# Optimization experiments

Measured on AMD Instinct MI355X. Metric: run time of the kernel, lower is better.

Reference implementation:

```python
import jax, jax.numpy as jnp
import numpy as np

N_SAM, N_GEN, N_E = 10000, 20000, 1000000
D_SAM, D_GEN = 2000, 500
D0, H = 256, [256, 128, 64]
SLOPE = 0.25


def _glorot(key, shape):
    fan_in, fan_out = shape
    s = jnp.sqrt(2.0 / (fan_in + fan_out))
    return jax.random.normal(key, shape, dtype=jnp.float32) * s


def setup_inputs() -> dict:
    key = jax.random.key(0)
    ks = jax.random.split(key, 24)
    inp = {
        "sam_feat": jax.random.normal(ks[0], (N_SAM, D_SAM), dtype=jnp.float32),
        "gen_feat": jax.random.normal(ks[1], (N_GEN, D_GEN), dtype=jnp.float32),
        "src_sg": jax.random.randint(ks[2], (N_E,), 0, N_SAM, dtype=jnp.int32),
        "dst_sg": jax.random.randint(ks[3], (N_E,), 0, N_GEN, dtype=jnp.int32),
        "src_gs": jax.random.randint(ks[4], (N_E,), 0, N_GEN, dtype=jnp.int32),
        "dst_gs": jax.random.randint(ks[5], (N_E,), 0, N_SAM, dtype=jnp.int32),
        # input projections (LinearLayer, xavier init)
        "l1_W": _glorot(ks[6], (D_SAM, D0)), "l1_b": jnp.zeros((D0,), jnp.float32),
        "l2_W": _glorot(ks[7], (D_GEN, D0)), "l2_b": jnp.zeros((D0,), jnp.float32),
    }
    dims = [(D0, H[0]), (H[0], H[1]), (H[1], H[2])]
    k = 8
    for i, (di, do) in enumerate(dims, start=1):
        for rel in ("sg", "gs"):
            inp[f"W{i}_{rel}"] = _glorot(ks[k], (di, do)); k += 1
            inp[f"b{i}_{rel}"] = jnp.zeros((do,), jnp.float32)
    return inp


def _graph_conv(h_src, src, dst, n_src, n_dst, W, b):
    """DGL GraphConv with norm='both': D_dst^{-1/2} A D_src^{-1/2} h W + b."""
    ones = jnp.ones(src.shape, dtype=h_src.dtype)
    deg_out = jnp.clip(jax.ops.segment_sum(ones, src, num_segments=n_src), 1.0)
    deg_in = jnp.clip(jax.ops.segment_sum(ones, dst, num_segments=n_dst), 1.0)
    h = h_src * jax.lax.rsqrt(deg_out)[:, None]
    agg = jax.ops.segment_sum(h[src], dst, num_segments=n_dst)  # [n_dst, d]
    agg = agg * jax.lax.rsqrt(deg_in)[:, None]
    return agg @ W + b


def reference(sam_feat, gen_feat, src_sg, dst_sg, src_gs, dst_gs,
              l1_W, l1_b, l2_W, l2_b,
              W1_sg, b1_sg, W1_gs, b1_gs,
              W2_sg, b2_sg, W2_gs, b2_gs,
              W3_sg, b3_sg, W3_gs, b3_gs):
    h_sam = sam_feat @ l1_W + l1_b
    h_gen = gen_feat @ l2_W + l2_b
    layers = [(W1_sg, b1_sg, W1_gs, b1_gs),
              (W2_sg, b2_sg, W2_gs, b2_gs),
              (W3_sg, b3_sg, W3_gs, b3_gs)]
    for Wsg, bsg, Wgs, bgs in layers:
        # HeteroGraphConv(sum): dst 'gen' receives from sam_gen, dst 'sam' from gen_sam
        new_gen = _graph_conv(h_sam, src_sg, dst_sg, N_SAM, N_GEN, Wsg, bsg)
        new_sam = _graph_conv(h_gen, src_gs, dst_gs, N_GEN, N_SAM, Wgs, bgs)
        h_sam = jax.nn.leaky_relu(new_sam, SLOPE)  # dropout is identity in eval mode
        h_gen = jax.nn.leaky_relu(new_gen, SLOPE)
    return h_sam, h_gen
```

## Files before the change

### kernel.cpp

```cpp
#include <hip/hip_runtime.h>
#include <hip/hip_bf16.h>
#include <stdint.h>

#define N_SAM 10000
#define N_GEN 20000
#define DSAM  2000
#define DGEN  500
#define NB    32
#define NBNS  10240
#define SSPAN 2560
#define MP_SAM 10048
#define MP_GEN 20032

typedef __hip_bfloat16 bf16;
typedef short bf16x8 __attribute__((ext_vector_type(8)));
typedef float f32x4 __attribute__((ext_vector_type(4)));

__device__ __forceinline__ float bfbits2f(unsigned short u) {
    unsigned v = ((unsigned)u) << 16;
    return __builtin_bit_cast(float, v);
}
__device__ __forceinline__ unsigned short f2bfbits(float f) {
    bf16 h = __float2bfloat16(f);
    return __builtin_bit_cast(unsigned short, h);
}
__device__ __forceinline__ unsigned packbf2(float lo, float hi) {
    return ((unsigned)f2bfbits(lo)) | (((unsigned)f2bfbits(hi)) << 16);
}
__device__ __forceinline__ void addu(uint4 u, float* a) {
    a[0] += __builtin_bit_cast(float, u.x << 16);
    a[1] += __builtin_bit_cast(float, u.x & 0xffff0000u);
    a[2] += __builtin_bit_cast(float, u.y << 16);
    a[3] += __builtin_bit_cast(float, u.y & 0xffff0000u);
    a[4] += __builtin_bit_cast(float, u.z << 16);
    a[5] += __builtin_bit_cast(float, u.z & 0xffff0000u);
    a[6] += __builtin_bit_cast(float, u.w << 16);
    a[7] += __builtin_bit_cast(float, u.w & 0xffff0000u);
}
__device__ __forceinline__ void gload16(const unsigned short* g, unsigned short* l) {
    __builtin_amdgcn_global_load_lds(
        (const __attribute__((address_space(1))) void*)g,
        (__attribute__((address_space(3))) void*)l, 16, 0, 0);
}

__global__ __launch_bounds__(1024) void hist_count_kernel(
    const int* __restrict__ ssg, const int* __restrict__ dsg,
    const int* __restrict__ sgs, const int* __restrict__ dgs,
    unsigned* __restrict__ cs_ssg, unsigned* __restrict__ cs_dsg,
    unsigned* __restrict__ cs_sgs, unsigned* __restrict__ cs_dgs,
    int ne, int chunk) {
    __shared__ unsigned bins[NBNS];
    const int* arr; unsigned* counts; int lo, hi, nb;
    switch (blockIdx.y) {
        case 0:  arr = ssg; counts = cs_ssg; lo = 0;     hi = 10000; nb = 10000; break;
        case 1:  arr = dsg; counts = cs_dsg; lo = 0;     hi = 10240; nb = 20000; break;
        case 2:  arr = dsg; counts = cs_dsg; lo = 10240; hi = 20000; nb = 20000; break;
        case 3:  arr = sgs; counts = cs_sgs; lo = 0;     hi = 10240; nb = 20000; break;
        case 4:  arr = sgs; counts = cs_sgs; lo = 10240; hi = 20000; nb = 20000; break;
        default: arr = dgs; counts = cs_dgs; lo = 0;     hi = 10000; nb = 10000; break;
    }
    int span = hi - lo;
    for (int i = threadIdx.x; i < span; i += 1024) bins[i] = 0u;
    __syncthreads();
    int blk = blockIdx.x;
    int e0 = blk * chunk;
    int e1 = e0 + chunk; if (e1 > ne) e1 = ne;
    for (int e = e0 + threadIdx.x; e < e1; e += 1024) {
        int b = arr[e];
        if (b >= lo && b < hi) atomicAdd(&bins[b - lo], 1u);
    }
    __syncthreads();
    unsigned* out = counts + (size_t)blk * nb + lo;
    for (int i = threadIdx.x; i < span; i += 1024) out[i] = bins[i];
}

__global__ __launch_bounds__(256) void reduce_counts_kernel(
    const unsigned* __restrict__ cs_ssg, const unsigned* __restrict__ cs_dsg,
    const unsigned* __restrict__ cs_sgs, const unsigned* __restrict__ cs_dgs,
    unsigned* __restrict__ cnt_dsg, unsigned* __restrict__ cnt_dgs,
    float* __restrict__ rs_out_sam, float* __restrict__ rs_in_gen,
    float* __restrict__ rs_out_gen, float* __restrict__ rs_in_sam) {
    int i = blockIdx.x * 256 + threadIdx.x;
    int which = blockIdx.y;
    const unsigned* cs; int nb;
    switch (which) {
        case 0:  cs = cs_ssg; nb = 10000; break;
        case 1:  cs = cs_dsg; nb = 20000; break;
        case 2:  cs = cs_sgs; nb = 20000; break;
        default: cs = cs_dgs; nb = 10000; break;
    }
    if (i >= nb) return;
    unsigned s = 0;
    #pragma unroll 4
    for (int b = 0; b < NB; b++) s += cs[(size_t)b * nb + i];
    unsigned c = (s < 1u) ? 1u : s;
    float r = rsqrtf((float)c);
    if (which == 0)      { rs_out_sam[i] = r; }
    else if (which == 1) { cnt_dsg[i] = s; rs_in_gen[i] = r; }
    else if (which == 2) { rs_out_gen[i] = r; }
    else                 { cnt_dgs[i] = s; rs_in_sam[i] = r; }
}

__global__ __launch_bounds__(1024) void scan2_kernel(
    const unsigned* __restrict__ c0, unsigned* __restrict__ r0, int nA,
    const unsigned* __restrict__ c1, unsigned* __restrict__ r1, int nB) {
    const unsigned* cnt; unsigned* row; int n;
    if (blockIdx.x == 0) { cnt = c0; row = r0; n = nA; }
    else                 { cnt = c1; row = r1; n = nB; }
    __shared__ unsigned sdata[1024];
    __shared__ unsigned carry_s;
    int t = threadIdx.x;
    if (t == 0) carry_s = 0;
    __syncthreads();
    for (int base = 0; base < n; base += 1024) {
        int i = base + t;
        unsigned v = (i < n) ? cnt[i] : 0u;
        sdata[t] = v;
        __syncthreads();
        for (int off = 1; off < 1024; off <<= 1) {
            unsigned add = (t >= off) ? sdata[t - off] : 0u;
            __syncthreads();
            sdata[t] += add;
            __syncthreads();
        }
        unsigned incl = sdata[t];
        unsigned carry = carry_s;
        if (i < n) row[i] = carry + incl - v;
        __syncthreads();
        if (t == 1023) carry_s = carry + incl;
        __syncthreads();
    }
    if (t == 0) row[n] = carry_s;
}

__global__ __launch_bounds__(256) void cursor_kernel(
    const unsigned* __restrict__ cs_dsg, const unsigned* __restrict__ cs_dgs,
    const unsigned* __restrict__ row_sg, const unsigned* __restrict__ row_gs,
    unsigned* __restrict__ cur_sg_m, unsigned* __restrict__ cur_gs_m) {
    int i = blockIdx.x * 256 + threadIdx.x;
    const unsigned* cs; const unsigned* row; unsigned* cur; int nb;
    if (blockIdx.y == 0) { cs = cs_dsg; row = row_sg; cur = cur_sg_m; nb = 20000; }
    else                 { cs = cs_dgs; row = row_gs; cur = cur_gs_m; nb = 10000; }
    if (i >= nb) return;
    unsigned run = row[i];
    for (int b = 0; b < NB; b++) {
        cur[(size_t)b * nb + i] = run;
        run += cs[(size_t)b * nb + i];
    }
}

__global__ __launch_bounds__(1024) void scatter_sorted_kernel(
    const int* __restrict__ src_sg, const int* __restrict__ dst_sg,
    const int* __restrict__ src_gs, const int* __restrict__ dst_gs,
    const unsigned* __restrict__ cur_sg_m, const unsigned* __restrict__ cur_gs_m,
    int* __restrict__ col_sg, int* __restrict__ col_gs, int ne, int chunk) {
    __shared__ unsigned curs[SSPAN];
    int sl = blockIdx.y;
    const int* src; const int* dst; const unsigned* cmat; int* col; int lo, hi, nb;
    if (sl < 8) {
        src = src_sg; dst = dst_sg; cmat = cur_sg_m; col = col_sg; nb = 20000;
        lo = sl * SSPAN; hi = lo + SSPAN; if (hi > 20000) hi = 20000;
    } else {
        src = src_gs; dst = dst_gs; cmat = cur_gs_m; col = col_gs; nb = 10000;
        lo = (sl - 8) * SSPAN; hi = lo + SSPAN; if (hi > 10000) hi = 10000;
    }
    int span = hi - lo, blk = blockIdx.x;
    const unsigned* cin = cmat + (size_t)blk * nb + lo;
    for (int i = threadIdx.x; i < span; i += 1024) curs[i] = cin[i];
    __syncthreads();
    int e0 = blk * chunk;
    int e1 = e0 + chunk; if (e1 > ne) e1 = ne;
    for (int e = e0 + threadIdx.x; e < e1; e += 1024) {
        int d = dst[e];
        if (d >= lo && d < hi) {
            unsigned p = atomicAdd(&curs[d - lo], 1u);
            col[p] = src[e];
        }
    }
}

__global__ __launch_bounds__(256) void convert_feat_kernel(
    const float* __restrict__ src, unsigned short* __restrict__ dst,
    int M, int K, int Mp, int kshift) {
    const int Kp = 1 << kshift;
    size_t ng = ((size_t)Mp << kshift) >> 3;
    for (size_t gi = (size_t)blockIdx.x * 256 + threadIdx.x; gi < ng;
         gi += (size_t)gridDim.x * 256) {
        size_t o8 = gi << 3;
        int row = (int)(o8 >> kshift);
        int col = (int)(o8 & (size_t)(Kp - 1));
        uint4 out;
        if (row < M && col + 8 <= K) {
            const float* p = src + (size_t)row * K + col;
            float4 u0 = *reinterpret_cast<const float4*>(p);
            float4 u1 = *reinterpret_cast<const float4*>(p + 4);
            out.x = packbf2(u0.x, u0.y);
            out.y = packbf2(u0.z, u0.w);
            out.z = packbf2(u1.x, u1.y);
            out.w = packbf2(u1.z, u1.w);
        } else {
            unsigned short v[8];
            #pragma unroll
            for (int j = 0; j < 8; j++) {
                float f = 0.0f;
                if (row < M && col + j < K) f = src[(size_t)row * K + col + j];
                v[j] = f2bfbits(f);
            }
            out.x = ((unsigned)v[0]) | (((unsigned)v[1]) << 16);
            out.y = ((unsigned)v[2]) | (((unsigned)v[3]) << 16);
            out.z = ((unsigned)v[4]) | (((unsigned)v[5]) << 16);
            out.w = ((unsigned)v[6]) | (((unsigned)v[7]) << 16);
        }
        *reinterpret_cast<uint4*>(dst + o8) = out;
    }
}

__global__ __launch_bounds__(256) void zero_pad_kernel(
    unsigned short* __restrict__ p0, int n0,
    unsigned short* __restrict__ p1, int n1) {
    int i = blockIdx.x * 256 + threadIdx.x;
    if (i < n0) p0[i] = 0;
    if (i < n1) p1[i] = 0;
}

struct WDesc { const float* src; unsigned short* dst; int K, N, Kp; };
struct WPack { WDesc d[8]; };

__global__ __launch_bounds__(256) void transpose_weights_kernel(WPack p) {
    WDesc d = p.d[blockIdx.z];
    int n  = blockIdx.x * 32 + threadIdx.x;
    int kp = blockIdx.y * 8 + threadIdx.y;
    if (n >= d.N || kp >= d.Kp) return;
    float v = (kp < d.K) ? d.src[(size_t)kp * d.N + n] : 0.0f;
    d.dst[(size_t)n * d.Kp + kp] = f2bfbits(v);
}

__global__ __launch_bounds__(256) void gemm_bf16(
    const unsigned short* __restrict__ A, const unsigned short* __restrict__ BT,
    const float* __restrict__ bias, const float* __restrict__ rs,
    unsigned short* __restrict__ C, int M, int N, int Kp, int GX, int GY) {
    int bi = blockIdx.x;
    int xcd = bi & 7, g = bi >> 3;
    int ntile = g % GX;
    int mtile = (g / GX) * 8 + xcd;
    if (mtile >= GY) return;
    int m0 = mtile * 64, n0 = ntile * 64;

    __shared__ __attribute__((aligned(16))) unsigned short As[2][64 * 64];
    __shared__ __attribute__((aligned(16))) unsigned short Bs[2][64 * 64];

    int t = threadIdx.x;
    int lane = t & 63;
    int wave = t >> 6;
    int wm = (wave >> 1) * 32, wn = (wave & 1) * 32;
    int q = lane >> 4, mr = lane & 15;

    int r0 = t >> 3;
    int sw = ((t & 7) ^ (r0 & 7)) << 3;
    const unsigned short* a0 = A + (size_t)(m0 + r0) * Kp + sw;
    const unsigned short* b0 = BT + (size_t)(n0 + r0) * Kp + sw;
    const size_t rstep = (size_t)32 * Kp;
    unsigned short* asl0 = &As[0][t * 8];
    unsigned short* asl1 = &As[0][(256 + t) * 8];
    unsigned short* bsl0 = &Bs[0][t * 8];
    unsigned short* bsl1 = &Bs[0][(256 + t) * 8];
    const int bufoff = 64 * 64;

    f32x4 acc[2][2] = {};

    gload16(a0, asl0);
    gload16(a0 + rstep, asl1);
    gload16(b0, bsl0);
    gload16(b0 + rstep, bsl1);
    __syncthreads();

    int nt = Kp >> 6;
    for (int it = 0; it < nt; ++it) {
        int cur = it & 1;
        if (it + 1 < nt) {
            int k0 = (it + 1) << 6;
            int boff = (cur ^ 1) * bufoff;
            gload16(a0 + k0,         asl0 + boff);
            gload16(a0 + rstep + k0, asl1 + boff);
            gload16(b0 + k0,         bsl0 + boff);
            gload16(b0 + rstep + k0, bsl1 + boff);
        }
        #pragma unroll
        for (int kk = 0; kk < 64; kk += 32) {
            bf16x8 af[2], bfr[2];
            int cb = (kk >> 3) + q;
            #pragma unroll
            for (int i = 0; i < 2; i++) {
                int row = wm + i * 16 + mr;
                af[i] = *reinterpret_cast<const bf16x8*>(
                    &As[cur][row * 64 + ((cb ^ (row & 7)) << 3)]);
            }
            #pragma unroll
            for (int j = 0; j < 2; j++) {
                int row = wn + j * 16 + mr;
                bfr[j] = *reinterpret_cast<const bf16x8*>(
                    &Bs[cur][row * 64 + ((cb ^ (row & 7)) << 3)]);
            }
            #pragma unroll
            for (int i = 0; i < 2; i++)
                #pragma unroll
                for (int j = 0; j < 2; j++)
                    acc[i][j] = __builtin_amdgcn_mfma_f32_16x16x32_bf16(
                        af[i], bfr[j], acc[i][j], 0, 0, 0);
        }
        __syncthreads();
    }

    #pragma unroll
    for (int i = 0; i < 2; i++) {
        #pragma unroll
        for (int r = 0; r < 4; r++) {
            int row = m0 + wm + i * 16 + q * 4 + r;
            if (row >= M) continue;
            float sc = (rs != nullptr) ? rs[row] : 1.0f;
            #pragma unroll
            for (int j = 0; j < 2; j++) {
                int col = n0 + wn + j * 16 + mr;
                float v = acc[i][j][r];
                if (bias != nullptr) v += bias[col];
                v *= sc;
                C[(size_t)row * N + col] = f2bfbits(v);
            }
        }
    }
}

struct AggSide {
    const unsigned* rowptr; const int* col; const unsigned short* P;
    const float* rs_in; const float* bias; const float* rs_next;
    float* outF; unsigned short* outB; int n_dst;
};

template <int VPL, bool OUTBF>
__global__ __launch_bounds__(256) void agg_csr2_kernel(AggSide a, AggSide b, int nblkA) {
    const int D = VPL * 64;
    const int LPR = VPL * 8;
    const int R = 8 / VPL;
    int blk = blockIdx.x;
    AggSide s;
    if (blk < nblkA) { s = a; } else { s = b; blk -= nblkA; }
    int wave = threadIdx.x >> 6;
    int lane = threadIdx.x & 63;
    int sub = lane / LPR;
    int li  = lane % LPR;
    int r = blk * 4 + wave;
    if (r >= s.n_dst) return;

    const unsigned short* __restrict__ P = s.P;
    const int* __restrict__ col = s.col;
    unsigned e0 = s.rowptr[r], e1 = s.rowptr[r + 1];
    float ac0[8] = {}, ac1[8] = {}, ac2[8] = {}, ac3[8] = {};
    unsigned e = e0;
    for (; e + 4 * R <= e1; e += 4 * R) {
        int s0 = col[e + sub];
        int s1 = col[e + R + sub];
        int s2 = col[e + 2 * R + sub];
        int s3 = col[e + 3 * R + sub];
        uint4 u0 = *reinterpret_cast<const uint4*>(P + (size_t)s0 * D + li * 8);
        uint4 u1 = *reinterpret_cast<const uint4*>(P + (size_t)s1 * D + li * 8);
        uint4 u2 = *reinterpret_cast<const uint4*>(P + (size_t)s2 * D + li * 8);
        uint4 u3 = *reinterpret_cast<const uint4*>(P + (size_t)s3 * D + li * 8);
        addu(u0, ac0); addu(u1, ac1); addu(u2, ac2); addu(u3, ac3);
    }
    for (; e < e1; e += R) {
        unsigned idx = e + sub;
        if (idx < e1) {
            int s0 = col[idx];
            uint4 u = *reinterpret_cast<const uint4*>(P + (size_t)s0 * D + li * 8);
            addu(u, ac0);
        }
    }
    #pragma unroll
    for (int j = 0; j < 8; j++) ac0[j] += (ac1[j] + ac2[j]) + ac3[j];
    #pragma unroll
    for (int off = 32; off >= LPR; off >>= 1) {
        #pragma unroll
        for (int j = 0; j < 8; j++) ac0[j] += __shfl_down(ac0[j], off);
    }
    if (sub == 0) {
        float rsv = s.rs_in[r];
        float res[8];
        #pragma unroll
        for (int j = 0; j < 8; j++) {
            float v = ac0[j] * rsv + s.bias[li * 8 + j];
            res[j] = (v >= 0.f) ? v : 0.25f * v;
        }
        if constexpr (OUTBF) {
            float sn = s.rs_next[r];
            uint4 o;
            o.x = packbf2(res[0] * sn, res[1] * sn);
            o.y = packbf2(res[2] * sn, res[3] * sn);
            o.z = packbf2(res[4] * sn, res[5] * sn);
            o.w = packbf2(res[6] * sn, res[7] * sn);
            *reinterpret_cast<uint4*>(s.outB + (size_t)r * D + li * 8) = o;
        } else {
            float* op = s.outF + (size_t)r * D + li * 8;
            *reinterpret_cast<float4*>(op)     = make_float4(res[0], res[1], res[2], res[3]);
            *reinterpret_cast<float4*>(op + 4) = make_float4(res[4], res[5], res[6], res[7]);
        }
    }
}

extern "C" void kernel_launch(void* const* d_in, const int* in_sizes, int n_in,
                              void* d_out, int out_size, void* d_ws, size_t ws_size,
                              hipStream_t stream) {
    const float* sam_feat = (const float*)d_in[0];
    const float* gen_feat = (const float*)d_in[1];
    const int* src_sg = (const int*)d_in[2];
    const int* dst_sg = (const int*)d_in[3];
    const int* src_gs = (const int*)d_in[4];
    const int* dst_gs = (const int*)d_in[5];
    const float* l1W = (const float*)d_in[6];
    const float* l1b = (const float*)d_in[7];
    const float* l2W = (const float*)d_in[8];
    const float* l2b = (const float*)d_in[9];
    const float* Wsg[3] = {(const float*)d_in[10], (const float*)d_in[14], (const float*)d_in[18]};
    const float* bsg[3] = {(const float*)d_in[11], (const float*)d_in[15], (const float*)d_in[19]};
    const float* Wgs[3] = {(const float*)d_in[12], (const float*)d_in[16], (const float*)d_in[20]};
    const float* bgs[3] = {(const float*)d_in[13], (const float*)d_in[17], (const float*)d_in[21]};
    const int NE = in_sizes[2];
    const int CHUNK = (NE + NB - 1) / NB;

    char* base = (char*)d_ws;
    size_t off = 0;
    auto alloc = [&](size_t bytes) -> char* {
        char* p = base + off;
        off = (off + bytes + 255) & ~(size_t)255;
        return p;
    };
    unsigned* cs_ssg = (unsigned*)alloc((size_t)NB * N_SAM * 4);
    unsigned* cs_dsg = (unsigned*)alloc((size_t)NB * N_GEN * 4);
    unsigned* cs_sgs = (unsigned*)alloc((size_t)NB * N_GEN * 4);
    unsigned* cs_dgs = (unsigned*)alloc((size_t)NB * N_SAM * 4);
    unsigned* cnt_dsg = (unsigned*)alloc(N_GEN * 4);
    unsigned* cnt_dgs = (unsigned*)alloc(N_SAM * 4);
    unsigned* row_sg = (unsigned*)alloc((N_GEN + 1) * 4);
    unsigned* row_gs = (unsigned*)alloc((N_SAM + 1) * 4);
    unsigned* cur_sg_m = (unsigned*)alloc((size_t)NB * N_GEN * 4);
    unsigned* cur_gs_m = (unsigned*)alloc((size_t)NB * N_SAM * 4);
    float* rs_out_sam = (float*)alloc(N_SAM * 4);
    float* rs_in_sam  = (float*)alloc(N_SAM * 4);
    float* rs_out_gen = (float*)alloc(N_GEN * 4);
    float* rs_in_gen  = (float*)alloc(N_GEN * 4);
    int* col_sg = (int*)alloc((size_t)NE * 4);
    int* col_gs = (int*)alloc((size_t)NE * 4);
    unsigned short* hs = (unsigned short*)alloc((size_t)MP_SAM * 256 * 2);
    unsigned short* hg = (unsigned short*)alloc((size_t)MP_GEN * 256 * 2);
    unsigned short* ps = (unsigned short*)alloc((size_t)N_SAM * 256 * 2);
    unsigned short* pg = (unsigned short*)alloc((size_t)N_GEN * 256 * 2);
    const int KP1 = 2048, KP2 = 512;
    unsigned short* BT_l1 = (unsigned short*)alloc((size_t)256 * KP1 * 2);
    unsigned short* BT_l2 = (unsigned short*)alloc((size_t)256 * KP2 * 2);
    unsigned short* BT_sg[3], *BT_gs[3];
    const int LN[3] = {256, 128, 64};
    const int LK[3] = {256, 256, 128};
    for (int i = 0; i < 3; i++) {
        BT_sg[i] = (unsigned short*)alloc((size_t)LN[i] * LK[i] * 2);
        BT_gs[i] = (unsigned short*)alloc((size_t)LN[i] * LK[i] * 2);
    }
    unsigned short* A_sam = (unsigned short*)alloc((size_t)MP_SAM * KP1 * 2);
    unsigned short* A_gen = (unsigned short*)alloc((size_t)MP_GEN * KP2 * 2);
    (void)ws_size;

    hist_count_kernel<<<dim3(NB, 6), 1024, 0, stream>>>(
        src_sg, dst_sg, src_gs, dst_gs, cs_ssg, cs_dsg, cs_sgs, cs_dgs, NE, CHUNK);
    reduce_counts_kernel<<<dim3((N_GEN + 255) / 256, 4), 256, 0, stream>>>(
        cs_ssg, cs_dsg, cs_sgs, cs_dgs, cnt_dsg, cnt_dgs,
        rs_out_sam, rs_in_gen, rs_out_gen, rs_in_sam);
    scan2_kernel<<<2, 1024, 0, stream>>>(cnt_dsg, row_sg, N_GEN, cnt_dgs, row_gs, N_SAM);
    cursor_kernel<<<dim3((N_GEN + 255) / 256, 2), 256, 0, stream>>>(
        cs_dsg, cs_dgs, row_sg, row_gs, cur_sg_m, cur_gs_m);
    scatter_sorted_kernel<<<dim3(NB, 12), 1024, 0, stream>>>(
        src_sg, dst_sg, src_gs, dst_gs, cur_sg_m, cur_gs_m, col_sg, col_gs, NE, CHUNK);

    convert_feat_kernel<<<2048, 256, 0, stream>>>(sam_feat, A_sam, N_SAM, DSAM, MP_SAM, 11);
    convert_feat_kernel<<<1024, 256, 0, stream>>>(gen_feat, A_gen, N_GEN, DGEN, MP_GEN, 9);
    zero_pad_kernel<<<48, 256, 0, stream>>>(
        hs + (size_t)N_SAM * 256, (MP_SAM - N_SAM) * 256,
        hg + (size_t)N_GEN * 256, (MP_GEN - N_GEN) * 256);

    WPack wp;
    wp.d[0] = {l1W,    BT_l1,    DSAM, 256, KP1};
    wp.d[1] = {l2W,    BT_l2,    DGEN, 256, KP2};
    wp.d[2] = {Wsg[0], BT_sg[0], 256, 256, 256};
    wp.d[3] = {Wgs[0], BT_gs[0], 256, 256, 256};
    wp.d[4] = {Wsg[1], BT_sg[1], 256, 128, 256};
    wp.d[5] = {Wgs[1], BT_gs[1], 256, 128, 256};
    wp.d[6] = {Wsg[2], BT_sg[2], 128, 64, 128};
    wp.d[7] = {Wgs[2], BT_gs[2], 128, 64, 128};
    transpose_weights_kernel<<<dim3(8, KP1 / 8, 8), dim3(32, 8), 0, stream>>>(wp);

    dim3 blk(256);
    const int GY_SAM = (N_SAM + 63) / 64;
    const int GY_GEN = (N_GEN + 63) / 64;
    auto swgrid = [](int GX, int GY) { return 8 * GX * ((GY + 7) / 8); };
    const int NBA_GEN = (N_GEN + 3) / 4;
    const int NBA_SAM = (N_SAM + 3) / 4;

    gemm_bf16<<<swgrid(4, GY_SAM), blk, 0, stream>>>(
        A_sam, BT_l1, l1b, rs_out_sam, hs, N_SAM, 256, KP1, 4, GY_SAM);
    gemm_bf16<<<swgrid(4, GY_GEN), blk, 0, stream>>>(
        A_gen, BT_l2, l2b, rs_out_gen, hg, N_GEN, 256, KP2, 4, GY_GEN);

    gemm_bf16<<<swgrid(4, GY_SAM), blk, 0, stream>>>(
        hs, BT_sg[0], nullptr, nullptr, ps, N_SAM, 256, 256, 4, GY_SAM);
    gemm_bf16<<<swgrid(4, GY_GEN), blk, 0, stream>>>(
        hg, BT_gs[0], nullptr, nullptr, pg, N_GEN, 256, 256, 4, GY_GEN);
    {
        AggSide gside = {row_sg, col_sg, ps, rs_in_gen, bsg[0], rs_out_gen, nullptr, hg, N_GEN};
        AggSide sside = {row_gs, col_gs, pg, rs_in_sam, bgs[0], rs_out_sam, nullptr, hs, N_SAM};
        agg_csr2_kernel<4, true><<<NBA_GEN + NBA_SAM, blk, 0, stream>>>(gside, sside, NBA_GEN);
    }

    gemm_bf16<<<swgrid(2, GY_SAM), blk, 0, stream>>>(
        hs, BT_sg[1], nullptr, nullptr, ps, N_SAM, 128, 256, 2, GY_SAM);
    gemm_bf16<<<swgrid(2, GY_GEN), blk, 0, stream>>>(
        hg, BT_gs[1], nullptr, nullptr, pg, N_GEN, 128, 256, 2, GY_GEN);
    {
        AggSide gside = {row_sg, col_sg, ps, rs_in_gen, bsg[1], rs_out_gen, nullptr, hg, N_GEN};
        AggSide sside = {row_gs, col_gs, pg, rs_in_sam, bgs[1], rs_out_sam, nullptr, hs, N_SAM};
        agg_csr2_kernel<2, true><<<NBA_GEN + NBA_SAM, blk, 0, stream>>>(gside, sside, NBA_GEN);
    }

    gemm_bf16<<<swgrid(1, GY_SAM), blk, 0, stream>>>(
        hs, BT_sg[2], nullptr, nullptr, ps, N_SAM, 64, 128, 1, GY_SAM);
    gemm_bf16<<<swgrid(1, GY_GEN), blk, 0, stream>>>(
        hg, BT_gs[2], nullptr, nullptr, pg, N_GEN, 64, 128, 1, GY_GEN);
    float* out_sam = (float*)d_out;
    float* out_gen = out_sam + (size_t)N_SAM * 64;
    {
        AggSide gside = {row_sg, col_sg, ps, rs_in_gen, bsg[2], nullptr, out_gen, nullptr, N_GEN};
        AggSide sside = {row_gs, col_gs, pg, rs_in_sam, bgs[2], nullptr, out_sam, nullptr, N_SAM};
        agg_csr2_kernel<1, false><<<NBA_GEN + NBA_SAM, blk, 0, stream>>>(gside, sside, NBA_GEN);
    }
}
```

Baseline: 550.7 us.

## Partition aggregation into eight XCD-pinned tasks by row range and feature slice

```diff
diff --git a/kernel.cpp b/kernel.cpp
--- a/kernel.cpp
+++ b/kernel.cpp
@@ -330,78 +330,82 @@
     }
 }
 
-struct AggSide {
+struct AggTask {
     const unsigned* rowptr; const int* col; const unsigned short* P;
     const float* rs_in; const float* bias; const float* rs_next;
-    float* outF; unsigned short* outB; int n_dst;
+    void* out;
+    int row_begin; int row_end; int D; int d0; int lprs;
 };
-
-template <int VPL, bool OUTBF>
-__global__ __launch_bounds__(256) void agg_csr2_kernel(AggSide a, AggSide b, int nblkA) {
-    const int D = VPL * 64;
-    const int LPR = VPL * 8;
-    const int R = 8 / VPL;
-    int blk = blockIdx.x;
-    AggSide s;
-    if (blk < nblkA) { s = a; } else { s = b; blk -= nblkA; }
-    int wave = threadIdx.x >> 6;
+struct AggPack { AggTask t[8]; };
+
+template <bool OUTBF>
+__global__ __launch_bounds__(256) void agg_xcd_kernel(AggPack pk) {
+    int task = blockIdx.x & 7;
+    int lblk = blockIdx.x >> 3;
+    int nlb  = (int)gridDim.x >> 3;
+    AggTask t = pk.t[task];
     int lane = threadIdx.x & 63;
-    int sub = lane / LPR;
-    int li  = lane % LPR;
-    int r = blk * 4 + wave;
-    if (r >= s.n_dst) return;
-
-    const unsigned short* __restrict__ P = s.P;
-    const int* __restrict__ col = s.col;
-    unsigned e0 = s.rowptr[r], e1 = s.rowptr[r + 1];
-    float ac0[8] = {}, ac1[8] = {}, ac2[8] = {}, ac3[8] = {};
-    unsigned e = e0;
-    for (; e + 4 * R <= e1; e += 4 * R) {
-        int s0 = col[e + sub];
-        int s1 = col[e + R + sub];
-        int s2 = col[e + 2 * R + sub];
-        int s3 = col[e + 3 * R + sub];
-        uint4 u0 = *reinterpret_cast<const uint4*>(P + (size_t)s0 * D + li * 8);
-        uint4 u1 = *reinterpret_cast<const uint4*>(P + (size_t)s1 * D + li * 8);
-        uint4 u2 = *reinterpret_cast<const uint4*>(P + (size_t)s2 * D + li * 8);
-        uint4 u3 = *reinterpret_cast<const uint4*>(P + (size_t)s3 * D + li * 8);
-        addu(u0, ac0); addu(u1, ac1); addu(u2, ac2); addu(u3, ac3);
-    }
-    for (; e < e1; e += R) {
-        unsigned idx = e + sub;
-        if (idx < e1) {
-            int s0 = col[idx];
-            uint4 u = *reinterpret_cast<const uint4*>(P + (size_t)s0 * D + li * 8);
-            addu(u, ac0);
-        }
-    }
-    #pragma unroll
-    for (int j = 0; j < 8; j++) ac0[j] += (ac1[j] + ac2[j]) + ac3[j];
-    #pragma unroll
-    for (int off = 32; off >= LPR; off >>= 1) {
+    int wav  = threadIdx.x >> 6;
+    const int LPR = 1 << t.lprs;
+    const int R   = 64 >> t.lprs;
+    int sub = lane >> t.lprs;
+    int li  = lane & (LPR - 1);
+    const int D = t.D;
+    const unsigned short* __restrict__ P = t.P + t.d0 + li * 8;
+    const int* __restrict__ col = t.col;
+    const int R4 = R << 2;
+
+    for (int r = t.row_begin + lblk * 4 + wav; r < t.row_end; r += nlb * 4) {
+        unsigned e0 = t.rowptr[r], e1 = t.rowptr[r + 1];
+        float ac0[8] = {}, ac1[8] = {};
+        unsigned e = e0;
+        for (; e + (unsigned)R4 <= e1; e += R4) {
+            int s0 = col[e + sub];
+            int s1 = col[e + R + sub];
+            int s2 = col[e + 2 * R + sub];
+            int s3 = col[e + 3 * R + sub];
+            uint4 u0 = *reinterpret_cast<const uint4*>(P + (size_t)s0 * D);
+            uint4 u1 = *reinterpret_cast<const uint4*>(P + (size_t)s1 * D);
+            uint4 u2 = *reinterpret_cast<const uint4*>(P + (size_t)s2 * D);
+            uint4 u3 = *reinterpret_cast<const uint4*>(P + (size_t)s3 * D);
+            addu(u0, ac0); addu(u1, ac1); addu(u2, ac0); addu(u3, ac1);
+        }
+        for (; e < e1; e += R) {
+            unsigned idx = e + sub;
+            if (idx < e1) {
+                int s0 = col[idx];
+                uint4 u = *reinterpret_cast<const uint4*>(P + (size_t)s0 * D);
+                addu(u, ac0);
+            }
+        }
         #pragma unroll
-        for (int j = 0; j < 8; j++) ac0[j] += __shfl_down(ac0[j], off);
-    }
-    if (sub == 0) {
-        float rsv = s.rs_in[r];
-        float res[8];
-        #pragma unroll
-        for (int j = 0; j < 8; j++) {
-            float v = ac0[j] * rsv + s.bias[li * 8 + j];
-            res[j] = (v >= 0.f) ? v : 0.25f * v;
-        }
-        if constexpr (OUTBF) {
-            float sn = s.rs_next[r];
-            uint4 o;
-            o.x = packbf2(res[0] * sn, res[1] * sn);
-            o.y = packbf2(res[2] * sn, res[3] * sn);
-            o.z = packbf2(res[4] * sn, res[5] * sn);
-            o.w = packbf2(res[6] * sn, res[7] * sn);
-            *reinterpret_cast<uint4*>(s.outB + (size_t)r * D + li * 8) = o;
-        } else {
-            float* op = s.outF + (size_t)r * D + li * 8;
-            *reinterpret_cast<float4*>(op)     = make_float4(res[0], res[1], res[2], res[3]);
-            *reinterpret_cast<float4*>(op + 4) = make_float4(res[4], res[5], res[6], res[7]);
+        for (int j = 0; j < 8; j++) ac0[j] += ac1[j];
+        for (int off = 32; off >= LPR; off >>= 1) {
+            #pragma unroll
+            for (int j = 0; j < 8; j++) ac0[j] += __shfl_down(ac0[j], off);
+        }
+        if (sub == 0) {
+            float rsv = t.rs_in[r];
+            float res[8];
+            #pragma unroll
+            for (int j = 0; j < 8; j++) {
+                float v = ac0[j] * rsv + t.bias[t.d0 + li * 8 + j];
+                res[j] = (v >= 0.f) ? v : 0.25f * v;
+            }
+            if constexpr (OUTBF) {
+                float sn = t.rs_next[r];
+                uint4 o;
+                o.x = packbf2(res[0] * sn, res[1] * sn);
+                o.y = packbf2(res[2] * sn, res[3] * sn);
+                o.z = packbf2(res[4] * sn, res[5] * sn);
+                o.w = packbf2(res[6] * sn, res[7] * sn);
+                *reinterpret_cast<uint4*>(
+                    (unsigned short*)t.out + (size_t)r * D + t.d0 + li * 8) = o;
+            } else {
+                float* op = (float*)t.out + (size_t)r * D + t.d0 + li * 8;
+                *reinterpret_cast<float4*>(op)     = make_float4(res[0], res[1], res[2], res[3]);
+                *reinterpret_cast<float4*>(op + 4) = make_float4(res[4], res[5], res[6], res[7]);
+            }
         }
     }
 }
@@ -499,22 +503,36 @@
     const int GY_SAM = (N_SAM + 63) / 64;
     const int GY_GEN = (N_GEN + 63) / 64;
     auto swgrid = [](int GX, int GY) { return 8 * GX * ((GY + 7) / 8); };
-    const int NBA_GEN = (N_GEN + 3) / 4;
-    const int NBA_SAM = (N_SAM + 3) / 4;
+    const int AGG_GRID = 2048;
 
     gemm_bf16<<<swgrid(4, GY_SAM), blk, 0, stream>>>(
         A_sam, BT_l1, l1b, rs_out_sam, hs, N_SAM, 256, KP1, 4, GY_SAM);
     gemm_bf16<<<swgrid(4, GY_GEN), blk, 0, stream>>>(
         A_gen, BT_l2, l2b, rs_out_gen, hg, N_GEN, 256, KP2, 4, GY_GEN);
+
+    auto mk = [](const unsigned* rp, const int* cl, const unsigned short* P,
+                 const float* ri, const float* bi, const float* rn, void* out,
+                 int rb, int re, int D, int d0, int lprs) {
+        AggTask t; t.rowptr = rp; t.col = cl; t.P = P; t.rs_in = ri; t.bias = bi;
+        t.rs_next = rn; t.out = out; t.row_begin = rb; t.row_end = re;
+        t.D = D; t.d0 = d0; t.lprs = lprs; return t;
+    };
 
     gemm_bf16<<<swgrid(4, GY_SAM), blk, 0, stream>>>(
         hs, BT_sg[0], nullptr, nullptr, ps, N_SAM, 256, 256, 4, GY_SAM);
     gemm_bf16<<<swgrid(4, GY_GEN), blk, 0, stream>>>(
         hg, BT_gs[0], nullptr, nullptr, pg, N_GEN, 256, 256, 4, GY_GEN);
     {
-        AggSide gside = {row_sg, col_sg, ps, rs_in_gen, bsg[0], rs_out_gen, nullptr, hg, N_GEN};
-        AggSide sside = {row_gs, col_gs, pg, rs_in_sam, bgs[0], rs_out_sam, nullptr, hs, N_SAM};
-        agg_csr2_kernel<4, true><<<NBA_GEN + NBA_SAM, blk, 0, stream>>>(gside, sside, NBA_GEN);
+        AggPack p;
+        p.t[0] = mk(row_sg, col_sg, ps, rs_in_gen, bsg[0], rs_out_gen, hg, 0, 10000, 256,   0, 4);
+        p.t[1] = mk(row_sg, col_sg, ps, rs_in_gen, bsg[0], rs_out_gen, hg, 10000, 20000, 256, 0, 4);
+        p.t[2] = mk(row_sg, col_sg, ps, rs_in_gen, bsg[0], rs_out_gen, hg, 0, 10000, 256, 128, 4);
+        p.t[3] = mk(row_sg, col_sg, ps, rs_in_gen, bsg[0], rs_out_gen, hg, 10000, 20000, 256, 128, 4);
+        p.t[4] = mk(row_gs, col_gs, pg, rs_in_sam, bgs[0], rs_out_sam, hs, 0, 10000, 256,   0, 3);
+        p.t[5] = mk(row_gs, col_gs, pg, rs_in_sam, bgs[0], rs_out_sam, hs, 0, 10000, 256,  64, 3);
+        p.t[6] = mk(row_gs, col_gs, pg, rs_in_sam, bgs[0], rs_out_sam, hs, 0, 10000, 256, 128, 3);
+        p.t[7] = mk(row_gs, col_gs, pg, rs_in_sam, bgs[0], rs_out_sam, hs, 0, 10000, 256, 192, 3);
+        agg_xcd_kernel<true><<<AGG_GRID, blk, 0, stream>>>(p);
     }
 
     gemm_bf16<<<swgrid(2, GY_SAM), blk, 0, stream>>>(
@@ -522,9 +540,16 @@
     gemm_bf16<<<swgrid(2, GY_GEN), blk, 0, stream>>>(
         hg, BT_gs[1], nullptr, nullptr, pg, N_GEN, 128, 256, 2, GY_GEN);
     {
-        AggSide gside = {row_sg, col_sg, ps, rs_in_gen, bsg[1], rs_out_gen, nullptr, hg, N_GEN};
-        AggSide sside = {row_gs, col_gs, pg, rs_in_sam, bgs[1], rs_out_sam, nullptr, hs, N_SAM};
-        agg_csr2_kernel<2, true><<<NBA_GEN + NBA_SAM, blk, 0, stream>>>(gside, sside, NBA_GEN);
+        AggPack p;
+        p.t[0] = mk(row_sg, col_sg, ps, rs_in_gen, bsg[1], rs_out_gen, hg, 0, 5000, 128, 0, 4);
+        p.t[1] = mk(row_sg, col_sg, ps, rs_in_gen, bsg[1], rs_out_gen, hg, 5000, 10000, 128, 0, 4);
+        p.t[2] = mk(row_sg, col_sg, ps, rs_in_gen, bsg[1], rs_out_gen, hg, 10000, 15000, 128, 0, 4);
+        p.t[3] = mk(row_sg, col_sg, ps, rs_in_gen, bsg[1], rs_out_gen, hg, 15000, 20000, 128, 0, 4);
+        p.t[4] = mk(row_gs, col_gs, pg, rs_in_sam, bgs[1], rs_out_sam, hs, 0, 5000, 128,  0, 3);
+        p.t[5] = mk(row_gs, col_gs, pg, rs_in_sam, bgs[1], rs_out_sam, hs, 5000, 10000, 128, 0, 3);
+        p.t[6] = mk(row_gs, col_gs, pg, rs_in_sam, bgs[1], rs_out_sam, hs, 0, 5000, 128, 64, 3);
+        p.t[7] = mk(row_gs, col_gs, pg, rs_in_sam, bgs[1], rs_out_sam, hs, 5000, 10000, 128, 64, 3);
+        agg_xcd_kernel<true><<<AGG_GRID, blk, 0, stream>>>(p);
     }
 
     gemm_bf16<<<swgrid(1, GY_SAM), blk, 0, stream>>>(
@@ -534,8 +559,15 @@
     float* out_sam = (float*)d_out;
     float* out_gen = out_sam + (size_t)N_SAM * 64;
     {
-        AggSide gside = {row_sg, col_sg, ps, rs_in_gen, bsg[2], nullptr, out_gen, nullptr, N_GEN};
-        AggSide sside = {row_gs, col_gs, pg, rs_in_sam, bgs[2], nullptr, out_sam, nullptr, N_SAM};
-        agg_csr2_kernel<1, false><<<NBA_GEN + NBA_SAM, blk, 0, stream>>>(gside, sside, NBA_GEN);
-    }
-}
+        AggPack p;
+        p.t[0] = mk(row_sg, col_sg, ps, rs_in_gen, bsg[2], nullptr, out_gen, 0, 5000, 64, 0, 3);
+        p.t[1] = mk(row_sg, col_sg, ps, rs_in_gen, bsg[2], nullptr, out_gen, 5000, 10000, 64, 0, 3);
+        p.t[2] = mk(row_sg, col_sg, ps, rs_in_gen, bsg[2], nullptr, out_gen, 10000, 15000, 64, 0, 3);
+        p.t[3] = mk(row_sg, col_sg, ps, rs_in_gen, bsg[2], nullptr, out_gen, 15000, 20000, 64, 0, 3);
+        p.t[4] = mk(row_gs, col_gs, pg, rs_in_sam, bgs[2], nullptr, out_sam, 0, 2500, 64, 0, 3);
+        p.t[5] = mk(row_gs, col_gs, pg, rs_in_sam, bgs[2], nullptr, out_sam, 2500, 5000, 64, 0, 3);
+        p.t[6] = mk(row_gs, col_gs, pg, rs_in_sam, bgs[2], nullptr, out_sam, 5000, 7500, 64, 0, 3);
+        p.t[7] = mk(row_gs, col_gs, pg, rs_in_sam, bgs[2], nullptr, out_sam, 7500, 10000, 64, 0, 3);
+        agg_xcd_kernel<false><<<AGG_GRID, blk, 0, stream>>>(p);
+    }
+}
```

Result: faster. 525.7 us (-4.5%).
